# Optimization experiments

Measured on AMD Instinct MI355X. Metric: run time of the kernel, lower is better.

## Reference

```python
import jax, jax.numpy as jnp
import numpy as np

N = 100000       # nodes
E = 1600000      # edges
F_IN = 128       # input features
HID = 64         # hidden dim
CLS = 16         # classes


def setup_inputs() -> dict:
    key = jax.random.key(0)
    k = jax.random.split(key, 6)
    x = jax.random.normal(k[0], (N, F_IN), dtype=jnp.float32)
    src = jax.random.randint(k[1], (E,), 0, N, dtype=jnp.int32)
    dst = jax.random.randint(k[2], (E,), 0, N, dtype=jnp.int32)
    edge_index = jnp.stack([src, dst], axis=0)
    W1 = jax.random.normal(k[3], (F_IN, HID), dtype=jnp.float32) * (1.0 / np.sqrt(F_IN))
    b1 = jnp.zeros((HID,), dtype=jnp.float32)
    W2 = jax.random.normal(k[4], (HID, CLS), dtype=jnp.float32) * (1.0 / np.sqrt(HID))
    b2 = jnp.zeros((CLS,), dtype=jnp.float32)
    return {"x": x, "edge_index": edge_index, "W1": W1, "b1": b1, "W2": W2, "b2": b2}


def gcn_conv(x, W, b, src, dst, n_nodes):
    # GCNConv(normalize=True): h = W x; out_i = sum_{j->i} h_j / sqrt(d_i d_j) + h_i / d_i + b
    # (self-loops added with weight 1; deg includes the self-loop)
    h = x @ W                                             # [N, out]
    ones = jnp.ones(src.shape[0], dtype=x.dtype)
    deg = jax.ops.segment_sum(ones, dst, num_segments=n_nodes) + 1.0   # [N]
    dinv = deg ** -0.5
    norm = dinv[src] * dinv[dst]                          # [E]
    msg = h[src] * norm[:, None]                          # [E, out] gather
    out = jax.ops.segment_sum(msg, dst, num_segments=n_nodes)          # scatter-add
    out = out + h * (1.0 / deg)[:, None] + b              # self-loop term + bias
    return out


def reference(x, edge_index, W1, b1, W2, b2):
    src, dst = edge_index[0], edge_index[1]
    n = x.shape[0]
    h = jax.nn.relu(gcn_conv(x, W1, b1, src, dst, n))
    # dropout(p=0.5) is identity in eval mode
    h = jax.nn.relu(gcn_conv(h, W2, b2, src, dst, n))
    return jax.nn.log_softmax(h, axis=-1)
```

## Files before the change

### kernel.cpp

```cpp
#include <hip/hip_runtime.h>
#include <hip/hip_bf16.h>


typedef unsigned short u16;
typedef __attribute__((ext_vector_type(8))) short short8;
typedef __attribute__((ext_vector_type(4))) float f32x4;

#define CAP 4096

__device__ __forceinline__ float bf2f(u16 u) {
  return __uint_as_float(((unsigned int)u) << 16);
}
__device__ __forceinline__ u16 f2bf(float f) {
  unsigned int u = __float_as_uint(f);
  u += 0x7fffu + ((u >> 16) & 1u);
  return (u16)(u >> 16);
}

__global__ __launch_bounds__(512) void kpartc(
    const int* __restrict__ src, const int* __restrict__ dst,
    int* __restrict__ cursor, int* __restrict__ etmp,
    const void* __restrict__ W1r, const void* __restrict__ b1r,
    const void* __restrict__ W2r, const void* __restrict__ b2r,
    u16* __restrict__ W1b, float* __restrict__ b1f, u16* __restrict__ W2b,
    float* __restrict__ b2f, int* __restrict__ mode, int E, int NB) {
  __shared__ int hist[1024], basep[1024];
  __shared__ float red[8];
  __shared__ int smode;
  int tid = threadIdx.x;

  if (blockIdx.x == 0) {
    const u16* w = (const u16*)W1r;
    float mx = 0.f;
    for (int i = tid; i < 8192; i += 512) {
      float av = fabsf(bf2f(w[i]));
      if (!(av <= 1e6f)) av = 3e38f;
      mx = fmaxf(mx, av);
    }
    #pragma unroll
    for (int off = 32; off >= 1; off >>= 1) mx = fmaxf(mx, __shfl_xor(mx, off, 64));
    if ((tid & 63) == 0) red[tid >> 6] = mx;
    __syncthreads();
    if (tid == 0) {
      float m2 = 0.f;
      #pragma unroll
      for (int wv = 0; wv < 8; ++wv) m2 = fmaxf(m2, red[wv]);
      smode = (m2 > 1e6f) ? 1 : 0;
      mode[0] = smode;
    }
    __syncthreads();
    int m = smode;
    for (int i = tid; i < 8192; i += 512)
      W1b[i] = m ? f2bf(((const float*)W1r)[i]) : ((const u16*)W1r)[i];
    for (int i = tid; i < 1024; i += 512)
      W2b[i] = m ? f2bf(((const float*)W2r)[i]) : ((const u16*)W2r)[i];
    if (tid < 64) b1f[tid] = m ? ((const float*)b1r)[tid] : bf2f(((const u16*)b1r)[tid]);
    if (tid < 16) b2f[tid] = m ? ((const float*)b2r)[tid] : bf2f(((const u16*)b2r)[tid]);
    return;
  }

  for (int i = tid; i < 1024; i += 512) hist[i] = 0;
  __syncthreads();
  int e0 = (blockIdx.x - 1) * 8192 + tid * 16;
  int pk[16], off[16], cb[16];
  if (e0 + 15 < E) {
    int4 s4[4], d4[4];
    #pragma unroll
    for (int u = 0; u < 4; ++u) {
      s4[u] = ((const int4*)(src + e0))[u];
      d4[u] = ((const int4*)(dst + e0))[u];
    }
    const int* sp = (const int*)s4;
    const int* dp = (const int*)d4;
    #pragma unroll
    for (int k = 0; k < 16; ++k) {
      int s = sp[k], d = dp[k];
      cb[k] = d >> 7;
      pk[k] = (s << 7) | (d & 127);
      off[k] = atomicAdd(&hist[cb[k]], 1);
    }
  } else {
    #pragma unroll
    for (int k = 0; k < 16; ++k) {
      int e = e0 + k;
      cb[k] = -1;
      if (e < E) {
        int s = src[e], d = dst[e];
        cb[k] = d >> 7;
        pk[k] = (s << 7) | (d & 127);
        off[k] = atomicAdd(&hist[cb[k]], 1);
      }
    }
  }
  __syncthreads();
  for (int i = tid; i < NB; i += 512)
    if (hist[i]) basep[i] = atomicAdd(&cursor[i], hist[i]);
  __syncthreads();
  if (e0 + 15 < E) {
    #pragma unroll
    for (int k = 0; k < 16; ++k)
      etmp[cb[k] * CAP + basep[cb[k]] + off[k]] = pk[k];
  } else {
    #pragma unroll
    for (int k = 0; k < 16; ++k)
      if (cb[k] >= 0) etmp[cb[k] * CAP + basep[cb[k]] + off[k]] = pk[k];
  }
}

__global__ __launch_bounds__(512) void kgemm1f(
    const void* __restrict__ xraw, const u16* __restrict__ W1b,
    const int* __restrict__ mode, const int* __restrict__ etmp,
    const int* __restrict__ cursor, float* __restrict__ dinv,
    u16* __restrict__ h1s, int N) {
  __shared__ int hist[128];
  __shared__ float sdinv[128];
  int tid = threadIdx.x;
  int bk = blockIdx.x;
  int base = bk * CAP;
  int cnt = cursor[bk];
  int node0 = bk << 7;

  if (tid < 128) hist[tid] = 0;
  __syncthreads();
  for (int i = tid; i < cnt; i += 512)
    atomicAdd(&hist[etmp[base + i] & 127], 1);
  __syncthreads();
  if (tid < 128) {
    float dv = rsqrtf((float)(hist[tid] + 1));
    sdinv[tid] = dv;
    int nd = node0 + tid;
    if (nd < N) dinv[nd] = dv;
  }
  __syncthreads();

  int mflag = mode[0];
  int lane = tid & 63, wv = tid >> 6;
  int m = lane & 15, q = lane >> 4;
  int row0 = node0 + wv * 16;

  short8 bfrag[4][4];
  for (int jb = 0; jb < 4; ++jb)
    for (int kb = 0; kb < 4; ++kb) {
      short8 f;
      #pragma unroll
      for (int j = 0; j < 8; ++j)
        f[j] = (short)W1b[(kb * 32 + q * 8 + j) * 64 + jb * 16 + m];
      bfrag[jb][kb] = f;
    }

  f32x4 acc[4];
  #pragma unroll
  for (int jb = 0; jb < 4; ++jb) acc[jb] = (f32x4){0.f, 0.f, 0.f, 0.f};

  int rowm = row0 + m;
  size_t rc = (size_t)((rowm < N) ? rowm : (N - 1));
  #pragma unroll
  for (int kb = 0; kb < 4; ++kb) {
    short8 a;
    if (mflag) {
      const float* xf = (const float*)xraw + rc * 128 + kb * 32 + q * 8;
      float4 u0 = ((const float4*)xf)[0];
      float4 u1 = ((const float4*)xf)[1];
      __hip_bfloat162 p0 = __float22bfloat162_rn(make_float2(u0.x, u0.y));
      __hip_bfloat162 p1 = __float22bfloat162_rn(make_float2(u0.z, u0.w));
      __hip_bfloat162 p2 = __float22bfloat162_rn(make_float2(u1.x, u1.y));
      __hip_bfloat162 p3 = __float22bfloat162_rn(make_float2(u1.z, u1.w));
      unsigned int w0 = *(const unsigned int*)&p0;
      unsigned int w1 = *(const unsigned int*)&p1;
      unsigned int w2 = *(const unsigned int*)&p2;
      unsigned int w3 = *(const unsigned int*)&p3;
      a[0] = (short)(w0 & 0xffff); a[1] = (short)(w0 >> 16);
      a[2] = (short)(w1 & 0xffff); a[3] = (short)(w1 >> 16);
      a[4] = (short)(w2 & 0xffff); a[5] = (short)(w2 >> 16);
      a[6] = (short)(w3 & 0xffff); a[7] = (short)(w3 >> 16);
    } else {
      a = *(const short8*)((const u16*)xraw + rc * 128 + kb * 32 + q * 8);
    }
    #pragma unroll
    for (int jb = 0; jb < 4; ++jb)
      acc[jb] = __builtin_amdgcn_mfma_f32_16x16x32_bf16(a, bfrag[jb][kb], acc[jb], 0, 0, 0);
  }

  #pragma unroll
  for (int r = 0; r < 4; ++r) {
    int rr = row0 + q * 4 + r;
    if (rr < N) {
      float dv = sdinv[wv * 16 + q * 4 + r];
      #pragma unroll
      for (int jb = 0; jb < 4; ++jb)
        h1s[(size_t)rr * 64 + jb * 16 + m] = f2bf(acc[jb][r] * dv);
    }
  }
}

__global__ __launch_bounds__(512) void kagg1f(
    const u16* __restrict__ h1s, const int* __restrict__ etmp,
    const int* __restrict__ cursor, const float* __restrict__ dinv,
    const float* __restrict__ b1f, const u16* __restrict__ W2b,
    int* __restrict__ esort, int2* __restrict__ rowse,
    u16* __restrict__ h2sb, int N) {
  __shared__ int eL[CAP];
  __shared__ int eS[CAP];
  __shared__ int hist[128], starts[128], curs[128];
  __shared__ float sdinv[128];

  int tid = threadIdx.x;
  int bk = blockIdx.x;
  int base = bk * CAP;
  int cnt = cursor[bk];
  int node0 = bk << 7;

  if (tid < 128) {
    hist[tid] = 0;
    int nd = node0 + tid;
    sdinv[tid] = (nd < N) ? dinv[nd] : 0.f;
  }
  __syncthreads();
  for (int i = tid; i < cnt; i += 512) {
    int pk = etmp[base + i];
    eL[i] = pk;
    atomicAdd(&hist[pk & 127], 1);
  }
  __syncthreads();
  if (tid < 64) {
    int v0 = hist[tid], v1 = hist[tid + 64];
    int s0 = v0;
    #pragma unroll
    for (int off = 1; off < 64; off <<= 1) {
      int t = __shfl_up(s0, off, 64);
      if (tid >= off) s0 += t;
    }
    int tot0 = __shfl(s0, 63, 64);
    int s1 = v1;
    #pragma unroll
    for (int off = 1; off < 64; off <<= 1) {
      int t = __shfl_up(s1, off, 64);
      if (tid >= off) s1 += t;
    }
    s1 += tot0;
    int e0x = s0 - v0, e1x = s1 - v1;
    starts[tid] = e0x;  curs[tid] = e0x;
    starts[tid + 64] = e1x;  curs[tid + 64] = e1x;
    int n0 = node0 + tid, n1 = n0 + 64;
    if (n0 < N) rowse[n0] = make_int2(base + e0x, base + e0x + v0);
    if (n1 < N) rowse[n1] = make_int2(base + e1x, base + e1x + v1);
  }
  __syncthreads();
  for (int i = tid; i < cnt; i += 512) {
    int pk = eL[i];
    int pos = atomicAdd(&curs[pk & 127], 1);
    int sidx = pk >> 7;
    eS[pos] = sidx;
    esort[base + pos] = sidx;
  }

  int lane = tid & 63, wv = tid >> 6;
  int m16 = lane & 15, q = lane >> 4;
  short8 bw0, bw1;
  #pragma unroll
  for (int j = 0; j < 8; ++j) {
    bw0[j] = (short)W2b[(q * 8 + j) * 16 + m16];
    bw1[j] = (short)W2b[(32 + q * 8 + j) * 16 + m16];
  }
  __syncthreads();

  float* rowsL = (float*)eL;
  const uint2* h1v = (const uint2*)h1s;
  int ql = m16;
  int wrow = wv * 4 + q;

  for (int pass = 0; pass < 4; ++pass) {
    int nl = pass * 32 + wv * 4 + q;
    int nd = node0 + nl;
    int cn = (nd < N) ? nd : node0;
    int rs = starts[nl], ke = rs + hist[nl];
    float a0 = 0.f, a1 = 0.f, a2 = 0.f, a3 = 0.f;
    int k = rs;
    for (; k + 8 <= ke; k += 8) {
      int sI[8];
      uint2 g[8];
      #pragma unroll
      for (int p = 0; p < 8; ++p) sI[p] = eS[k + p];
      #pragma unroll
      for (int p = 0; p < 8; ++p) g[p] = h1v[sI[p] * 16 + ql];
      #pragma unroll
      for (int p = 0; p < 8; ++p) {
        a0 += bf2f((u16)(g[p].x & 0xffff));
        a1 += bf2f((u16)(g[p].x >> 16));
        a2 += bf2f((u16)(g[p].y & 0xffff));
        a3 += bf2f((u16)(g[p].y >> 16));
      }
    }
    for (; k < ke; ++k) {
      int s = eS[k];
      uint2 g = h1v[s * 16 + ql];
      a0 += bf2f((u16)(g.x & 0xffff));
      a1 += bf2f((u16)(g.x >> 16));
      a2 += bf2f((u16)(g.y & 0xffff));
      a3 += bf2f((u16)(g.y >> 16));
    }
    uint2 sg = h1v[cn * 16 + ql];
    float dv = sdinv[nl];
    float4 bv = ((const float4*)b1f)[ql];
    float4 vr;
    vr.x = fmaxf(dv * (a0 + bf2f((u16)(sg.x & 0xffff))) + bv.x, 0.f);
    vr.y = fmaxf(dv * (a1 + bf2f((u16)(sg.x >> 16))) + bv.y, 0.f);
    vr.z = fmaxf(dv * (a2 + bf2f((u16)(sg.y & 0xffff))) + bv.z, 0.f);
    vr.w = fmaxf(dv * (a3 + bf2f((u16)(sg.y >> 16))) + bv.w, 0.f);

    *(float4*)&rowsL[wrow * 68 + 4 * ql] = vr;
    __builtin_amdgcn_wave_barrier();

    const float* ar = &rowsL[(wv * 4 + (m16 & 3)) * 68];
    bool rv = (m16 < 4);
    short8 af0, af1;
    #pragma unroll
    for (int j = 0; j < 8; ++j) {
      af0[j] = rv ? (short)f2bf(ar[q * 8 + j]) : (short)0;
      af1[j] = rv ? (short)f2bf(ar[32 + q * 8 + j]) : (short)0;
    }
    f32x4 c = (f32x4){0.f, 0.f, 0.f, 0.f};
    c = __builtin_amdgcn_mfma_f32_16x16x32_bf16(af0, bw0, c, 0, 0, 0);
    c = __builtin_amdgcn_mfma_f32_16x16x32_bf16(af1, bw1, c, 0, 0, 0);
    if (q == 0) {
      #pragma unroll
      for (int r = 0; r < 4; ++r) {
        int nl2 = pass * 32 + wv * 4 + r;
        int nd2 = node0 + nl2;
        if (nd2 < N) h2sb[nd2 * 16 + m16] = f2bf(c[r] * sdinv[nl2]);
      }
    }
    __builtin_amdgcn_wave_barrier();
  }
}

__global__ __launch_bounds__(256) void kagg2(
    const u16* __restrict__ h2sb, const int* __restrict__ esort,
    const int2* __restrict__ rowse, const float* __restrict__ dinv,
    const float* __restrict__ b2f, const int* __restrict__ mode,
    void* __restrict__ out, int n) {
  int mflag = mode[0];
  int tid = threadIdx.x;
  int lane = tid & 63, wv = tid >> 6;
  int oc = lane >> 3, ol = lane & 7;
  int hl = ol >> 2, fl = ol & 3;
  int node = blockIdx.x * 32 + wv * 8 + oc;
  if (node >= n) node = n - 1;
  int2 se = rowse[node];
  int beg = se.x, end = se.y;
  const uint2* h2v = (const uint2*)h2sb;
  uint2 sg = h2v[node * 4 + fl];
  float a0 = 0.f, a1 = 0.f, a2 = 0.f, a3 = 0.f;

  int k = beg;
  for (; k + 8 <= end; k += 8) {
    int i0 = esort[k + hl], i1 = esort[k + 2 + hl];
    int i2 = esort[k + 4 + hl], i3 = esort[k + 6 + hl];
    uint2 g0 = h2v[i0 * 4 + fl];
    uint2 g1 = h2v[i1 * 4 + fl];
    uint2 g2 = h2v[i2 * 4 + fl];
    uint2 g3 = h2v[i3 * 4 + fl];
    a0 += bf2f((u16)(g0.x & 0xffff)) + bf2f((u16)(g1.x & 0xffff))
        + bf2f((u16)(g2.x & 0xffff)) + bf2f((u16)(g3.x & 0xffff));
    a1 += bf2f((u16)(g0.x >> 16)) + bf2f((u16)(g1.x >> 16))
        + bf2f((u16)(g2.x >> 16)) + bf2f((u16)(g3.x >> 16));
    a2 += bf2f((u16)(g0.y & 0xffff)) + bf2f((u16)(g1.y & 0xffff))
        + bf2f((u16)(g2.y & 0xffff)) + bf2f((u16)(g3.y & 0xffff));
    a3 += bf2f((u16)(g0.y >> 16)) + bf2f((u16)(g1.y >> 16))
        + bf2f((u16)(g2.y >> 16)) + bf2f((u16)(g3.y >> 16));
  }
  for (; k < end; k += 2) {
    int e = k + hl;
    bool valid = e < end;
    uint2 g = h2v[esort[valid ? e : (end - 1)] * 4 + fl];
    if (valid) {
      a0 += bf2f((u16)(g.x & 0xffff));  a1 += bf2f((u16)(g.x >> 16));
      a2 += bf2f((u16)(g.y & 0xffff));  a3 += bf2f((u16)(g.y >> 16));
    }
  }
  a0 += __shfl_xor(a0, 4, 8);  a1 += __shfl_xor(a1, 4, 8);
  a2 += __shfl_xor(a2, 4, 8);  a3 += __shfl_xor(a3, 4, 8);

  float dv = dinv[node];
  float4 bv = ((const float4*)b2f)[fl];
  float v0 = fmaxf(dv * (a0 + bf2f((u16)(sg.x & 0xffff))) + bv.x, 0.f);
  float v1 = fmaxf(dv * (a1 + bf2f((u16)(sg.x >> 16))) + bv.y, 0.f);
  float v2 = fmaxf(dv * (a2 + bf2f((u16)(sg.y & 0xffff))) + bv.z, 0.f);
  float v3 = fmaxf(dv * (a3 + bf2f((u16)(sg.y >> 16))) + bv.w, 0.f);

  float m = fmaxf(fmaxf(v0, v1), fmaxf(v2, v3));
  m = fmaxf(m, __shfl_xor(m, 1, 4));
  m = fmaxf(m, __shfl_xor(m, 2, 4));
  float ex = __expf(v0 - m) + __expf(v1 - m) + __expf(v2 - m) + __expf(v3 - m);
  ex += __shfl_xor(ex, 1, 4);
  ex += __shfl_xor(ex, 2, 4);
  float lg = __logf(ex);
  float r0 = v0 - m - lg, r1 = v1 - m - lg;
  float r2 = v2 - m - lg, r3 = v3 - m - lg;
  if (hl == 0) {
    if (mflag) {
      ((float4*)out)[(size_t)node * 4 + fl] = make_float4(r0, r1, r2, r3);
    } else {
      uint2 o;
      o.x = (unsigned int)f2bf(r0) | ((unsigned int)f2bf(r1) << 16);
      o.y = (unsigned int)f2bf(r2) | ((unsigned int)f2bf(r3) << 16);
      ((uint2*)out)[(size_t)node * 4 + fl] = o;
    }
  }
}

extern "C" void kernel_launch(void* const* d_in, const int* in_sizes, int n_in,
                              void* d_out, int out_size, void* d_ws, size_t ws_size,
                              hipStream_t stream) {
  const void* x  = d_in[0];
  const int* ei  = (const int*)d_in[1];
  const void* W1 = d_in[2];
  const void* b1 = d_in[3];
  const void* W2 = d_in[4];
  const void* b2 = d_in[5];

  const int N = in_sizes[0] / 128;
  const int E = in_sizes[1] / 2;
  const int* src = ei;
  const int* dst = ei + E;
  const int NB = (N + 127) >> 7;

  char* ws = (char*)d_ws;
  size_t off = 0;
  auto alloc = [&](size_t bytes) -> char* {
    char* p = ws + off;
    off = (off + bytes + 255) & ~(size_t)255;
    return p;
  };
  u16*   h1s    = (u16*)  alloc((size_t)N * 64 * 2);
  u16*   h2sb   = (u16*)  alloc((size_t)N * 16 * 2);
  int*   etmp   = (int*)  alloc((size_t)NB * CAP * 4);
  int*   esort  = (int*)  alloc((size_t)NB * CAP * 4);
  int2*  rowse  = (int2*) alloc((size_t)N * 8);
  float* dinv   = (float*)alloc((size_t)N * 4);
  int*   cursor = (int*)  alloc((size_t)NB * 4);
  u16*   W1b    = (u16*)  alloc(8192 * 2);
  u16*   W2b    = (u16*)  alloc(1024 * 2);
  float* b1f    = (float*)alloc(64 * 4);
  float* b2f    = (float*)alloc(16 * 4);
  int*   mode   = (int*)  alloc(4);

  hipMemsetAsync(cursor, 0, (size_t)NB * 4, stream);

  int pblocks = (E + 8191) / 8192;
  kpartc<<<pblocks + 1, 512, 0, stream>>>(src, dst, cursor, etmp,
                                          W1, b1, W2, b2,
                                          W1b, b1f, W2b, b2f, mode, E, NB);
  kgemm1f<<<NB, 512, 0, stream>>>(x, W1b, mode, etmp, cursor, dinv, h1s, N);
  kagg1f<<<NB, 512, 0, stream>>>(h1s, etmp, cursor, dinv, b1f, W2b,
                                 esort, rowse, h2sb, N);
  kagg2<<<(N + 31) / 32, 256, 0, stream>>>(h2sb, esort, rowse, dinv, b2f, mode,
                                           d_out, N);
}
```

Measured before the change: 194.7 us.

## Move CSR sort into gemm kernel and regrid layer-1 aggregation per node

The per-bucket counting sort that builds esort and rowse moves out of the layer-1 aggregation kernel and into the GEMM kernel, which already loads the bucket's edges and builds the histogram. The aggregation kernel is rebuilt as a lightweight 256-thread kernel over 64 nodes per block. Each node is served by 8 lanes that fetch 16-byte bf16 rows, with edge indices prefetched and shared through shuffles. This drops the 32 KB of LDS and the serial per-bucket sort phase, which should raise occupancy and parallelism for the gather. The cost is a larger GEMM kernel with an extra LDS buffer, and the aggregation now reads the sorted edge list back from global memory.

```diff
diff --git a/kernel.cpp b/kernel.cpp
--- a/kernel.cpp
+++ b/kernel.cpp
@@ -15,6 +15,12 @@
   unsigned int u = __float_as_uint(f);
   u += 0x7fffu + ((u >> 16) & 1u);
   return (u16)(u >> 16);
+}
+__device__ __forceinline__ float blo(unsigned int u) {
+  return __uint_as_float(u << 16);
+}
+__device__ __forceinline__ float bhi(unsigned int u) {
+  return __uint_as_float(u & 0xffff0000u);
 }
 
 __global__ __launch_bounds__(512) void kpartc(
@@ -111,8 +117,10 @@
     const void* __restrict__ xraw, const u16* __restrict__ W1b,
     const int* __restrict__ mode, const int* __restrict__ etmp,
     const int* __restrict__ cursor, float* __restrict__ dinv,
-    u16* __restrict__ h1s, int N) {
-  __shared__ int hist[128];
+    u16* __restrict__ h1s, int* __restrict__ esort, int2* __restrict__ rowse,
+    int N) {
+  __shared__ int eL[CAP];
+  __shared__ int hist[128], curs[128];
   __shared__ float sdinv[128];
   int tid = threadIdx.x;
   int bk = blockIdx.x;
@@ -122,8 +130,11 @@
 
   if (tid < 128) hist[tid] = 0;
   __syncthreads();
-  for (int i = tid; i < cnt; i += 512)
-    atomicAdd(&hist[etmp[base + i] & 127], 1);
+  for (int i = tid; i < cnt; i += 512) {
+    int pk = etmp[base + i];
+    eL[i] = pk;
+    atomicAdd(&hist[pk & 127], 1);
+  }
   __syncthreads();
   if (tid < 128) {
     float dv = rsqrtf((float)(hist[tid] + 1));
@@ -131,7 +142,35 @@
     int nd = node0 + tid;
     if (nd < N) dinv[nd] = dv;
   }
-  __syncthreads();
+  if (tid < 64) {
+    int v0 = hist[tid], v1 = hist[tid + 64];
+    int s0 = v0;
+    #pragma unroll
+    for (int off = 1; off < 64; off <<= 1) {
+      int t = __shfl_up(s0, off, 64);
+      if (tid >= off) s0 += t;
+    }
+    int tot0 = __shfl(s0, 63, 64);
+    int s1 = v1;
+    #pragma unroll
+    for (int off = 1; off < 64; off <<= 1) {
+      int t = __shfl_up(s1, off, 64);
+      if (tid >= off) s1 += t;
+    }
+    s1 += tot0;
+    int e0x = s0 - v0, e1x = s1 - v1;
+    curs[tid] = e0x;
+    curs[tid + 64] = e1x;
+    int n0 = node0 + tid, n1 = n0 + 64;
+    if (n0 < N) rowse[n0] = make_int2(base + e0x, base + e0x + v0);
+    if (n1 < N) rowse[n1] = make_int2(base + e1x, base + e1x + v1);
+  }
+  __syncthreads();
+  for (int i = tid; i < cnt; i += 512) {
+    int pk = eL[i];
+    int pos = atomicAdd(&curs[pk & 127], 1);
+    esort[base + pos] = pk >> 7;
+  }
 
   int mflag = mode[0];
   int lane = tid & 63, wv = tid >> 6;
@@ -193,68 +232,80 @@
   }
 }
 
-__global__ __launch_bounds__(512) void kagg1f(
-    const u16* __restrict__ h1s, const int* __restrict__ etmp,
-    const int* __restrict__ cursor, const float* __restrict__ dinv,
+__global__ __launch_bounds__(256) void kagg1f(
+    const u16* __restrict__ h1s, const int* __restrict__ esort,
+    const int2* __restrict__ rowse, const float* __restrict__ dinv,
     const float* __restrict__ b1f, const u16* __restrict__ W2b,
-    int* __restrict__ esort, int2* __restrict__ rowse,
     u16* __restrict__ h2sb, int N) {
-  __shared__ int eL[CAP];
-  __shared__ int eS[CAP];
-  __shared__ int hist[128], starts[128], curs[128];
-  __shared__ float sdinv[128];
-
+  __shared__ __align__(16) u16 sA[4][16 * 72];
+  __shared__ float sdv[4][16];
   int tid = threadIdx.x;
-  int bk = blockIdx.x;
-  int base = bk * CAP;
-  int cnt = cursor[bk];
-  int node0 = bk << 7;
-
-  if (tid < 128) {
-    hist[tid] = 0;
-    int nd = node0 + tid;
-    sdinv[tid] = (nd < N) ? dinv[nd] : 0.f;
-  }
-  __syncthreads();
-  for (int i = tid; i < cnt; i += 512) {
-    int pk = etmp[base + i];
-    eL[i] = pk;
-    atomicAdd(&hist[pk & 127], 1);
-  }
-  __syncthreads();
-  if (tid < 64) {
-    int v0 = hist[tid], v1 = hist[tid + 64];
-    int s0 = v0;
-    #pragma unroll
-    for (int off = 1; off < 64; off <<= 1) {
-      int t = __shfl_up(s0, off, 64);
-      if (tid >= off) s0 += t;
-    }
-    int tot0 = __shfl(s0, 63, 64);
-    int s1 = v1;
-    #pragma unroll
-    for (int off = 1; off < 64; off <<= 1) {
-      int t = __shfl_up(s1, off, 64);
-      if (tid >= off) s1 += t;
-    }
-    s1 += tot0;
-    int e0x = s0 - v0, e1x = s1 - v1;
-    starts[tid] = e0x;  curs[tid] = e0x;
-    starts[tid + 64] = e1x;  curs[tid + 64] = e1x;
-    int n0 = node0 + tid, n1 = n0 + 64;
-    if (n0 < N) rowse[n0] = make_int2(base + e0x, base + e0x + v0);
-    if (n1 < N) rowse[n1] = make_int2(base + e1x, base + e1x + v1);
-  }
-  __syncthreads();
-  for (int i = tid; i < cnt; i += 512) {
-    int pk = eL[i];
-    int pos = atomicAdd(&curs[pk & 127], 1);
-    int sidx = pk >> 7;
-    eS[pos] = sidx;
-    esort[base + pos] = sidx;
-  }
-
   int lane = tid & 63, wv = tid >> 6;
+  int o = lane >> 3, fl = lane & 7;
+  int wbase = blockIdx.x * 64 + wv * 16;
+
+  const uint4* __restrict__ h1v4 = (const uint4*)h1s;
+
+  #pragma unroll
+  for (int sub = 0; sub < 2; ++sub) {
+    int nloc = sub * 8 + o;
+    int node = wbase + nloc;
+    int cn = (node < N) ? node : (N - 1);
+    int2 se = (node < N) ? rowse[node] : make_int2(0, 0);
+    int beg = se.x, end = se.y;
+    float a0 = 0.f, a1 = 0.f, a2 = 0.f, a3 = 0.f;
+    float a4 = 0.f, a5 = 0.f, a6 = 0.f, a7 = 0.f;
+
+    int k = beg;
+    int myi = (k + 8 <= end) ? esort[k + fl] : 0;
+    while (k + 8 <= end) {
+      int cur = myi;
+      if (k + 16 <= end) myi = esort[k + 8 + fl];
+      uint4 g[8];
+      #pragma unroll
+      for (int p = 0; p < 8; ++p) {
+        int s = __shfl(cur, (o << 3) + p, 64);
+        g[p] = h1v4[s * 8 + fl];
+      }
+      #pragma unroll
+      for (int p = 0; p < 8; ++p) {
+        a0 += blo(g[p].x); a1 += bhi(g[p].x);
+        a2 += blo(g[p].y); a3 += bhi(g[p].y);
+        a4 += blo(g[p].z); a5 += bhi(g[p].z);
+        a6 += blo(g[p].w); a7 += bhi(g[p].w);
+      }
+      k += 8;
+    }
+    for (; k < end; ++k) {
+      int s = esort[k];
+      uint4 g = h1v4[s * 8 + fl];
+      a0 += blo(g.x); a1 += bhi(g.x);
+      a2 += blo(g.y); a3 += bhi(g.y);
+      a4 += blo(g.z); a5 += bhi(g.z);
+      a6 += blo(g.w); a7 += bhi(g.w);
+    }
+
+    uint4 sg = h1v4[cn * 8 + fl];
+    float dv = dinv[cn];
+    float4 bva = ((const float4*)b1f)[fl * 2];
+    float4 bvb = ((const float4*)b1f)[fl * 2 + 1];
+    float v0 = fmaxf(dv * (a0 + blo(sg.x)) + bva.x, 0.f);
+    float v1 = fmaxf(dv * (a1 + bhi(sg.x)) + bva.y, 0.f);
+    float v2 = fmaxf(dv * (a2 + blo(sg.y)) + bva.z, 0.f);
+    float v3 = fmaxf(dv * (a3 + bhi(sg.y)) + bva.w, 0.f);
+    float v4 = fmaxf(dv * (a4 + blo(sg.z)) + bvb.x, 0.f);
+    float v5 = fmaxf(dv * (a5 + bhi(sg.z)) + bvb.y, 0.f);
+    float v6 = fmaxf(dv * (a6 + blo(sg.w)) + bvb.z, 0.f);
+    float v7 = fmaxf(dv * (a7 + bhi(sg.w)) + bvb.w, 0.f);
+    uint4 st;
+    st.x = (unsigned int)f2bf(v0) | ((unsigned int)f2bf(v1) << 16);
+    st.y = (unsigned int)f2bf(v2) | ((unsigned int)f2bf(v3) << 16);
+    st.z = (unsigned int)f2bf(v4) | ((unsigned int)f2bf(v5) << 16);
+    st.w = (unsigned int)f2bf(v6) | ((unsigned int)f2bf(v7) << 16);
+    *(uint4*)&sA[wv][nloc * 72 + fl * 8] = st;
+    if (fl == 0) sdv[wv][nloc] = dv;
+  }
+
   int m16 = lane & 15, q = lane >> 4;
   short8 bw0, bw1;
   #pragma unroll
@@ -262,75 +313,19 @@
     bw0[j] = (short)W2b[(q * 8 + j) * 16 + m16];
     bw1[j] = (short)W2b[(32 + q * 8 + j) * 16 + m16];
   }
-  __syncthreads();
-
-  float* rowsL = (float*)eL;
-  const uint2* h1v = (const uint2*)h1s;
-  int ql = m16;
-  int wrow = wv * 4 + q;
-
-  for (int pass = 0; pass < 4; ++pass) {
-    int nl = pass * 32 + wv * 4 + q;
-    int nd = node0 + nl;
-    int cn = (nd < N) ? nd : node0;
-    int rs = starts[nl], ke = rs + hist[nl];
-    float a0 = 0.f, a1 = 0.f, a2 = 0.f, a3 = 0.f;
-    int k = rs;
-    for (; k + 8 <= ke; k += 8) {
-      int sI[8];
-      uint2 g[8];
-      #pragma unroll
-      for (int p = 0; p < 8; ++p) sI[p] = eS[k + p];
-      #pragma unroll
-      for (int p = 0; p < 8; ++p) g[p] = h1v[sI[p] * 16 + ql];
-      #pragma unroll
-      for (int p = 0; p < 8; ++p) {
-        a0 += bf2f((u16)(g[p].x & 0xffff));
-        a1 += bf2f((u16)(g[p].x >> 16));
-        a2 += bf2f((u16)(g[p].y & 0xffff));
-        a3 += bf2f((u16)(g[p].y >> 16));
-      }
-    }
-    for (; k < ke; ++k) {
-      int s = eS[k];
-      uint2 g = h1v[s * 16 + ql];
-      a0 += bf2f((u16)(g.x & 0xffff));
-      a1 += bf2f((u16)(g.x >> 16));
-      a2 += bf2f((u16)(g.y & 0xffff));
-      a3 += bf2f((u16)(g.y >> 16));
-    }
-    uint2 sg = h1v[cn * 16 + ql];
-    float dv = sdinv[nl];
-    float4 bv = ((const float4*)b1f)[ql];
-    float4 vr;
-    vr.x = fmaxf(dv * (a0 + bf2f((u16)(sg.x & 0xffff))) + bv.x, 0.f);
-    vr.y = fmaxf(dv * (a1 + bf2f((u16)(sg.x >> 16))) + bv.y, 0.f);
-    vr.z = fmaxf(dv * (a2 + bf2f((u16)(sg.y & 0xffff))) + bv.z, 0.f);
-    vr.w = fmaxf(dv * (a3 + bf2f((u16)(sg.y >> 16))) + bv.w, 0.f);
-
-    *(float4*)&rowsL[wrow * 68 + 4 * ql] = vr;
-    __builtin_amdgcn_wave_barrier();
-
-    const float* ar = &rowsL[(wv * 4 + (m16 & 3)) * 68];
-    bool rv = (m16 < 4);
-    short8 af0, af1;
-    #pragma unroll
-    for (int j = 0; j < 8; ++j) {
-      af0[j] = rv ? (short)f2bf(ar[q * 8 + j]) : (short)0;
-      af1[j] = rv ? (short)f2bf(ar[32 + q * 8 + j]) : (short)0;
-    }
-    f32x4 c = (f32x4){0.f, 0.f, 0.f, 0.f};
-    c = __builtin_amdgcn_mfma_f32_16x16x32_bf16(af0, bw0, c, 0, 0, 0);
-    c = __builtin_amdgcn_mfma_f32_16x16x32_bf16(af1, bw1, c, 0, 0, 0);
-    if (q == 0) {
-      #pragma unroll
-      for (int r = 0; r < 4; ++r) {
-        int nl2 = pass * 32 + wv * 4 + r;
-        int nd2 = node0 + nl2;
-        if (nd2 < N) h2sb[nd2 * 16 + m16] = f2bf(c[r] * sdinv[nl2]);
-      }
-    }
-    __builtin_amdgcn_wave_barrier();
+  __builtin_amdgcn_wave_barrier();
+
+  const u16* ar = &sA[wv][m16 * 72];
+  short8 af0 = *(const short8*)(ar + q * 8);
+  short8 af1 = *(const short8*)(ar + 32 + q * 8);
+  f32x4 c = (f32x4){0.f, 0.f, 0.f, 0.f};
+  c = __builtin_amdgcn_mfma_f32_16x16x32_bf16(af0, bw0, c, 0, 0, 0);
+  c = __builtin_amdgcn_mfma_f32_16x16x32_bf16(af1, bw1, c, 0, 0, 0);
+  #pragma unroll
+  for (int r = 0; r < 4; ++r) {
+    int nloc2 = q * 4 + r;
+    int nd2 = wbase + nloc2;
+    if (nd2 < N) h2sb[(size_t)nd2 * 16 + m16] = f2bf(c[r] * sdv[wv][nloc2]);
   }
 }
 
@@ -451,9 +446,10 @@
   kpartc<<<pblocks + 1, 512, 0, stream>>>(src, dst, cursor, etmp,
                                           W1, b1, W2, b2,
                                           W1b, b1f, W2b, b2f, mode, E, NB);
-  kgemm1f<<<NB, 512, 0, stream>>>(x, W1b, mode, etmp, cursor, dinv, h1s, N);
-  kagg1f<<<NB, 512, 0, stream>>>(h1s, etmp, cursor, dinv, b1f, W2b,
-                                 esort, rowse, h2sb, N);
+  kgemm1f<<<NB, 512, 0, stream>>>(x, W1b, mode, etmp, cursor, dinv, h1s,
+                                  esort, rowse, N);
+  kagg1f<<<(N + 63) / 64, 256, 0, stream>>>(h1s, esort, rowse, dinv, b1f, W2b,
+                                            h2sb, N);
   kagg2<<<(N + 31) / 32, 256, 0, stream>>>(h2sb, esort, rowse, dinv, b2f, mode,
                                            d_out, N);
 }
```

Result: no change. 198.4 us (+1.9%).
